# Optimization experiments

Hardware: AMD Instinct MI355X
Metric: run time of the kernel (lower is better)

## Reference

```python
import jax, jax.numpy as jnp
import numpy as np

DIM = 512
NUM_HEADS = 8
HEAD_DIM = DIM // NUM_HEADS
SOFT_CAP = 50.0
EPS = 1e-6
ROPE_BASE = 10000.0


def _rope_cos_sin(T):
    inv_freq = 1.0 / (ROPE_BASE ** (jnp.arange(0, HEAD_DIM, 2, dtype=jnp.float32) / HEAD_DIM))
    t = jnp.arange(T, dtype=jnp.float32)
    freqs = jnp.einsum('t,f->tf', t, inv_freq)            # (T, HEAD_DIM//2)
    emb = jnp.concatenate([freqs, freqs], axis=-1)         # (T, HEAD_DIM)
    return jnp.cos(emb), jnp.sin(emb)


def _rotate_half(x):
    x1, x2 = jnp.split(x, 2, axis=-1)
    return jnp.concatenate([-x2, x1], axis=-1)


def _apply_rope(x, cos, sin):
    # x: (B,H,T,hd); cos/sin: (T,hd) broadcast over B,H
    return x * cos + _rotate_half(x) * sin


def _rmsnorm(x, g):
    var = jnp.mean(jnp.square(x), axis=-1, keepdims=True)
    return x * jax.lax.rsqrt(var + EPS) * g


def setup_inputs() -> dict:
    key = jax.random.key(0)
    ks = jax.random.split(key, 7)
    B, T = 256, 256
    s = 1.0 / np.sqrt(DIM)
    return {
        'x': jax.random.normal(ks[0], (B, T, DIM), dtype=jnp.float32),
        'wq': jax.random.normal(ks[1], (DIM, DIM), dtype=jnp.float32) * s,
        'wk': jax.random.normal(ks[2], (DIM, DIM), dtype=jnp.float32) * s,
        'wv': jax.random.normal(ks[3], (DIM, DIM), dtype=jnp.float32) * s,
        'wo': jax.random.normal(ks[4], (DIM, DIM), dtype=jnp.float32) * s,
        'gq': jnp.ones((HEAD_DIM,), dtype=jnp.float32),
        'gk': jnp.ones((HEAD_DIM,), dtype=jnp.float32),
    }


def reference(x, wq, wk, wv, wo, gq, gk):
    B, T, D = x.shape
    H, hd = NUM_HEADS, HEAD_DIM
    scale = hd ** -0.5

    def proj(w):
        return jnp.einsum('btd,ed->bte', x, w).reshape(B, T, H, hd).transpose(0, 2, 1, 3)

    q = proj(wq)  # (B,H,T,hd)
    k = proj(wk)
    v = proj(wv)

    q = _rmsnorm(q, gq)
    k = _rmsnorm(k, gk)

    cos, sin = _rope_cos_sin(T)
    q = _apply_rope(q, cos, sin)
    k = _apply_rope(k, cos, sin)

    attn = jnp.einsum('bhqd,bhkd->bhqk', q, k) * scale
    attn = SOFT_CAP * jnp.tanh(attn / SOFT_CAP)
    causal = jnp.tril(jnp.ones((T, T), dtype=bool))
    attn = jnp.where(causal, attn, -jnp.inf)
    attn = jax.nn.softmax(attn.astype(jnp.float32), axis=-1).astype(v.dtype)

    out = jnp.einsum('bhqk,bhkd->bhqd', attn, v)
    out = out.transpose(0, 2, 1, 3).reshape(B, T, D)
    return jnp.einsum('btd,ed->bte', out, wo)
```

## Files before the change

kernel.cpp:

```cpp
#include <hip/hip_runtime.h>
#include <cstdint>
#include <cstddef>

#define B_   256
#define T_   256
#define D_   512
#define H_   8
#define HD_  64
#define BT_  65536
#define KDIM 512

typedef __bf16 bf16x8_t __attribute__((ext_vector_type(8)));
typedef __bf16 bf16x4_t __attribute__((ext_vector_type(4)));
typedef float  f32x4_t  __attribute__((ext_vector_type(4)));

__device__ __forceinline__ void gload16(const void* gp, void* lp) {
  __builtin_amdgcn_global_load_lds(
      (const __attribute__((address_space(1))) void*)gp,
      (__attribute__((address_space(3))) void*)lp, 16, 0, 0);
}

#define BAR()   __builtin_amdgcn_s_barrier()
#define SCB()   __builtin_amdgcn_sched_barrier(0)
#define LGKM0() asm volatile("s_waitcnt lgkmcnt(0)" ::: "memory")

__global__ __launch_bounds__(256) void prep(
    const float* __restrict__ x,
    const float* __restrict__ wq, const float* __restrict__ wk,
    const float* __restrict__ wv, const float* __restrict__ wo,
    __bf16* __restrict__ xb, __bf16* __restrict__ wb,
    float* __restrict__ rc, float* __restrict__ rs) {
  const int b = blockIdx.x;
  if (b < 2048) {
    for (size_t i = (size_t)b * 256 + threadIdx.x; i < 8388608UL; i += 524288UL) {
      f32x4_t v = *(const f32x4_t*)&x[i * 4];
      bf16x4_t o;
      o[0] = (__bf16)v[0]; o[1] = (__bf16)v[1]; o[2] = (__bf16)v[2]; o[3] = (__bf16)v[3];
      *(bf16x4_t*)&xb[i * 4] = o;
    }
  } else if (b < 2304) {
    for (int i = (b - 2048) * 256 + threadIdx.x; i < 262144; i += 65536) {
      int which = i >> 16;
      int off   = (i & 65535) * 4;
      const float* src = (which == 0) ? wq : (which == 1) ? wk : (which == 2) ? wv : wo;
      f32x4_t v = *(const f32x4_t*)&src[off];
      bf16x4_t o;
      o[0] = (__bf16)v[0]; o[1] = (__bf16)v[1]; o[2] = (__bf16)v[2]; o[3] = (__bf16)v[3];
      *(bf16x4_t*)&wb[(size_t)which * 262144 + off] = o;
    }
  } else {
    int idx = (b - 2304) * 256 + threadIdx.x;
    if (idx < T_ * 32) {
      int t = idx >> 5, j = idx & 31;
      float inv = powf(10000.f, -(float)j * (1.0f / 32.0f));
      float a = (float)t * inv;
      rc[idx] = cosf(a);
      rs[idx] = sinf(a);
    }
  }
}

template <int MODE>
__global__ __launch_bounds__(256, 2) void gemm256(
    const __bf16* __restrict__ A, const __bf16* __restrict__ W,
    void* __restrict__ outp) {
  __shared__ __bf16 lds[32768];
  const int tid = threadIdx.x;
  const int lane = tid & 63, w = tid >> 6;
  const int wm = w >> 1, wn = w & 1;
  const int l15 = lane & 15, lg = lane >> 4;
  const int swl = l15 & 7;

  const int cpx = gridDim.x >> 3;
  const int swz = (blockIdx.x & 7) * cpx + (blockIdx.x >> 3);
  int m_idx, bz, bx;
  if (MODE == 0) {
    m_idx = swz / 12;
    const int rem = swz - m_idx * 12;
    bz = rem >> 2;
    bx = rem & 3;
  } else {
    m_idx = swz >> 2;
    bz = 0;
    bx = swz & 3;
  }
  const int m0 = m_idx * 128, n0 = bx * 128;

  const __bf16* Ag = A + (size_t)m0 * KDIM;
  const __bf16* Bg = W + (size_t)bz * (KDIM * KDIM) + (size_t)n0 * KDIM;
  const int srow = tid >> 3;
  const int scol = (((tid & 7) ^ ((tid >> 3) & 7)) * 8);

#define STAGE(J) do {                                                        \
    const int T__ = (J) >> 2, r__ = (J) & 3;                                 \
    const int h__ = r__ >> 1;                                                \
    const int isB__ = (r__ == 1 || r__ == 2);                                \
    const size_t grow__ = (size_t)(h__ * 64 + srow) * KDIM + T__ * 64 + scol; \
    const __bf16* gp__ = isB__ ? (Bg + grow__) : (Ag + grow__);              \
    __bf16* lp__ = &lds[(T__ & 1) * 16384 + isB__ * 8192 + (h__ * 64 + w * 8) * 64]; \
    gload16(gp__, lp__);                                                     \
    gload16(gp__ + 32 * KDIM, lp__ + 32 * 64);                               \
  } while (0)

  f32x4_t acc[4][4];
#pragma unroll
  for (int i = 0; i < 4; i++)
#pragma unroll
    for (int j = 0; j < 4; j++) acc[i][j] = (f32x4_t){0.f, 0.f, 0.f, 0.f};

  bf16x8_t a0[2][2], a1[2][2], b0[2][2], b1[2][2];

#define PH_A(P, STJ) do {                                                    \
    const int ab__ = (P) * 16384;                                            \
    _Pragma("unroll") for (int i = 0; i < 2; i++)                            \
      _Pragma("unroll") for (int s = 0; s < 2; s++)                          \
        a0[i][s] = *(const bf16x8_t*)&lds[ab__ + (wm * 32 + i * 16 + l15) * 64 + (((s * 4 + lg) ^ swl) << 3)]; \
    _Pragma("unroll") for (int j = 0; j < 2; j++)                            \
      _Pragma("unroll") for (int s = 0; s < 2; s++)                          \
        b0[j][s] = *(const bf16x8_t*)&lds[ab__ + 8192 + (wn * 32 + j * 16 + l15) * 64 + (((s * 4 + lg) ^ swl) << 3)]; \
    if ((STJ) >= 0) STAGE(STJ);                                              \
    SCB(); BAR(); LGKM0(); SCB();                                            \
    __builtin_amdgcn_s_setprio(1);                                           \
    _Pragma("unroll") for (int i = 0; i < 2; i++)                            \
      _Pragma("unroll") for (int j = 0; j < 2; j++) {                        \
        acc[i][j] = __builtin_amdgcn_mfma_f32_16x16x32_bf16(a0[i][0], b0[j][0], acc[i][j], 0, 0, 0); \
        acc[i][j] = __builtin_amdgcn_mfma_f32_16x16x32_bf16(a0[i][1], b0[j][1], acc[i][j], 0, 0, 0); \
      }                                                                      \
    __builtin_amdgcn_s_setprio(0); SCB(); BAR();                             \
  } while (0)

#define PH_B(P, STJ) do {                                                    \
    const int ab__ = (P) * 16384;                                            \
    _Pragma("unroll") for (int j = 0; j < 2; j++)                            \
      _Pragma("unroll") for (int s = 0; s < 2; s++)                          \
        b1[j][s] = *(const bf16x8_t*)&lds[ab__ + 8192 + (64 + wn * 32 + j * 16 + l15) * 64 + (((s * 4 + lg) ^ swl) << 3)]; \
    if ((STJ) >= 0) STAGE(STJ);                                              \
    SCB(); BAR(); LGKM0(); SCB();                                            \
    __builtin_amdgcn_s_setprio(1);                                           \
    _Pragma("unroll") for (int i = 0; i < 2; i++)                            \
      _Pragma("unroll") for (int j = 0; j < 2; j++) {                        \
        acc[i][j + 2] = __builtin_amdgcn_mfma_f32_16x16x32_bf16(a0[i][0], b1[j][0], acc[i][j + 2], 0, 0, 0); \
        acc[i][j + 2] = __builtin_amdgcn_mfma_f32_16x16x32_bf16(a0[i][1], b1[j][1], acc[i][j + 2], 0, 0, 0); \
      }                                                                      \
    __builtin_amdgcn_s_setprio(0); SCB(); BAR();                             \
  } while (0)

#define PH_C(P, STJ) do {                                                    \
    const int ab__ = (P) * 16384;                                            \
    _Pragma("unroll") for (int i = 0; i < 2; i++)                            \
      _Pragma("unroll") for (int s = 0; s < 2; s++)                          \
        a1[i][s] = *(const bf16x8_t*)&lds[ab__ + (64 + wm * 32 + i * 16 + l15) * 64 + (((s * 4 + lg) ^ swl) << 3)]; \
    if ((STJ) >= 0) STAGE(STJ);                                              \
    SCB(); BAR(); LGKM0(); SCB();                                            \
    __builtin_amdgcn_s_setprio(1);                                           \
    _Pragma("unroll") for (int i = 0; i < 2; i++)                            \
      _Pragma("unroll") for (int j = 0; j < 2; j++) {                        \
        acc[i + 2][j + 2] = __builtin_amdgcn_mfma_f32_16x16x32_bf16(a1[i][0], b1[j][0], acc[i + 2][j + 2], 0, 0, 0); \
        acc[i + 2][j + 2] = __builtin_amdgcn_mfma_f32_16x16x32_bf16(a1[i][1], b1[j][1], acc[i + 2][j + 2], 0, 0, 0); \
      }                                                                      \
    __builtin_amdgcn_s_setprio(0); SCB(); BAR();                             \
  } while (0)

#define PH_D(P, STJ, VM) do {                                                \
    if ((STJ) >= 0) STAGE(STJ);                                              \
    SCB(); BAR();                                                            \
    __builtin_amdgcn_s_setprio(1);                                           \
    _Pragma("unroll") for (int i = 0; i < 2; i++)                            \
      _Pragma("unroll") for (int j = 0; j < 2; j++) {                        \
        acc[i + 2][j] = __builtin_amdgcn_mfma_f32_16x16x32_bf16(a1[i][0], b0[j][0], acc[i + 2][j], 0, 0, 0); \
        acc[i + 2][j] = __builtin_amdgcn_mfma_f32_16x16x32_bf16(a1[i][1], b0[j][1], acc[i + 2][j], 0, 0, 0); \
      }                                                                      \
    __builtin_amdgcn_s_setprio(0);                                           \
    if ((VM) == 6) asm volatile("s_waitcnt vmcnt(6)" ::: "memory");          \
    else if ((VM) == 0) asm volatile("s_waitcnt vmcnt(0)" ::: "memory");     \
    SCB(); BAR();                                                            \
  } while (0)

  STAGE(0); STAGE(1); STAGE(2); STAGE(3); STAGE(4); STAGE(5); STAGE(6);
  asm volatile("s_waitcnt vmcnt(6)" ::: "memory");
  SCB(); BAR();

#pragma unroll 1
  for (int tp = 0; tp < 3; ++tp) {
    const int g0 = tp * 8;
    PH_A(0, g0 + 7);  PH_B(0, g0 + 8);  PH_C(0, g0 + 9);  PH_D(0, g0 + 10, 6);
    PH_A(1, g0 + 11); PH_B(1, g0 + 12); PH_C(1, g0 + 13); PH_D(1, g0 + 14, 6);
  }
  PH_A(0, 31); PH_B(0, -1); PH_C(0, -1); PH_D(0, -1, 0);
  PH_A(1, -1); PH_B(1, -1); PH_C(1, -1); PH_D(1, -1, -1);

#undef PH_A
#undef PH_B
#undef PH_C
#undef PH_D
#undef STAGE

#pragma unroll
  for (int i = 0; i < 4; i++) {
#pragma unroll
    for (int rr = 0; rr < 4; rr++) {
      const int m = m0 + (i >> 1) * 64 + wm * 32 + (i & 1) * 16 + lg * 4 + rr;
      if (MODE == 0) {
        __bf16* outz = (__bf16*)outp + (size_t)bz * ((size_t)BT_ * D_);
        const int bb = m >> 8, tt = m & 255;
        const size_t rbase = ((size_t)bb * H_) * T_ * HD_ + (size_t)tt * HD_;
#pragma unroll
        for (int j = 0; j < 4; j++) {
          const int c = n0 + (j >> 1) * 64 + wn * 32 + (j & 1) * 16 + l15;
          const int hh = c >> 6, dd = c & 63;
          outz[rbase + (size_t)hh * (T_ * HD_) + dd] = (__bf16)acc[i][j][rr];
        }
      } else {
        float* outf = (float*)outp;
#pragma unroll
        for (int j = 0; j < 4; j++) {
          const int c = n0 + (j >> 1) * 64 + wn * 32 + (j & 1) * 16 + l15;
          outf[(size_t)m * D_ + c] = acc[i][j][rr];
        }
      }
    }
  }
}

__global__ __launch_bounds__(512, 2) void attn_kernel(
    const __bf16* __restrict__ qb, const __bf16* __restrict__ kb,
    const __bf16* __restrict__ vb, __bf16* __restrict__ ob,
    const float* __restrict__ gq, const float* __restrict__ gk,
    const float* __restrict__ rc, const float* __restrict__ rs) {
  __shared__ __bf16 Kl[256 * 64];
  __shared__ __bf16 VT[64 * 256];
  __shared__ __bf16 Pl[8 * 16 * 64];
  const int bh = blockIdx.x;
  const __bf16* Qg = qb + (size_t)bh * (T_ * HD_);
  const __bf16* Kg = kb + (size_t)bh * (T_ * HD_);
  const __bf16* Vg = vb + (size_t)bh * (T_ * HD_);
  const int tid = threadIdx.x, lane = tid & 63, w = tid >> 6;
  const int bI = bh >> 3, hI = bh & 7;

#pragma unroll
  for (int p = 0; p < 4; p++) {
    const int t = p * 64 + (tid >> 3);
    const int a = tid & 7;
    const int d0 = a * 8;
    bf16x8_t kv = *(const bf16x8_t*)&Kg[t * HD_ + d0];
    float kf[8], ss = 0.f;
#pragma unroll
    for (int j = 0; j < 8; j++) { kf[j] = (float)kv[j]; ss += kf[j] * kf[j]; }
    ss += __shfl_xor(ss, 1); ss += __shfl_xor(ss, 2); ss += __shfl_xor(ss, 4);
    const float rn = rsqrtf(ss * 0.015625f + 1e-6f);
    const f32x4_t gk0 = *(const f32x4_t*)&gk[d0];
    const f32x4_t gk1 = *(const f32x4_t*)&gk[d0 + 4];
    float vn[8];
#pragma unroll
    for (int j = 0; j < 8; j++) vn[j] = kf[j] * rn * ((j < 4) ? gk0[j] : gk1[j - 4]);
    float pn[8];
#pragma unroll
    for (int j = 0; j < 8; j++) pn[j] = __shfl_xor(vn[j], 4);
    const int f0 = (a & 3) * 8;
    const f32x4_t c0 = *(const f32x4_t*)&rc[t * 32 + f0];
    const f32x4_t c1 = *(const f32x4_t*)&rc[t * 32 + f0 + 4];
    const f32x4_t s0 = *(const f32x4_t*)&rs[t * 32 + f0];
    const f32x4_t s1 = *(const f32x4_t*)&rs[t * 32 + f0 + 4];
    const float sg = (a < 4) ? -1.f : 1.f;
    bf16x8_t ko;
#pragma unroll
    for (int j = 0; j < 8; j++) {
      const float cc = (j < 4) ? c0[j] : c1[j - 4];
      const float sS = (j < 4) ? s0[j] : s1[j - 4];
      ko[j] = (__bf16)(vn[j] * cc + sg * pn[j] * sS);
    }
    *(bf16x8_t*)&Kl[t * 64 + (((a ^ (t & 7)) << 3))] = ko;
    bf16x8_t vv = *(const bf16x8_t*)&Vg[t * HD_ + d0];
#pragma unroll
    for (int j = 0; j < 8; j++) {
      const int row = d0 + j;
      const int rk = (row & 7) ^ ((row >> 3) & 7);
      VT[row * 256 + (((t >> 3) ^ rk) << 3) + (t & 7)] = vv[j];
    }
  }
  __syncthreads();

  const int l15 = lane & 15;
  const int lg = lane >> 4;
  const int sw = l15 & 7;
  const f32x4_t zero = {0.f, 0.f, 0.f, 0.f};
  const float C1 = 0.0072134752f;
  const float LOG2E = 1.44269504f;

  for (int half = 0; half < 2; half++) {
    const int qt = half ? (15 - w) : w;
    const int q0 = qt * 16;
    const int tq = q0 + l15;
    bf16x8_t q0r = *(const bf16x8_t*)&Qg[tq * HD_ + lg * 8];
    bf16x8_t q1r = *(const bf16x8_t*)&Qg[tq * HD_ + 32 + lg * 8];
    float qf0[8], qf1[8], qss = 0.f;
#pragma unroll
    for (int j = 0; j < 8; j++) {
      qf0[j] = (float)q0r[j]; qf1[j] = (float)q1r[j];
      qss += qf0[j] * qf0[j] + qf1[j] * qf1[j];
    }
    qss += __shfl_xor(qss, 16); qss += __shfl_xor(qss, 32);
    const float qrn = rsqrtf(qss * 0.015625f + 1e-6f);
    const f32x4_t gqa = *(const f32x4_t*)&gq[lg * 8];
    const f32x4_t gqb2 = *(const f32x4_t*)&gq[lg * 8 + 4];
    const f32x4_t gqc = *(const f32x4_t*)&gq[32 + lg * 8];
    const f32x4_t gqd = *(const f32x4_t*)&gq[32 + lg * 8 + 4];
    const f32x4_t qc0 = *(const f32x4_t*)&rc[tq * 32 + lg * 8];
    const f32x4_t qc1 = *(const f32x4_t*)&rc[tq * 32 + lg * 8 + 4];
    const f32x4_t qs0 = *(const f32x4_t*)&rs[tq * 32 + lg * 8];
    const f32x4_t qs1 = *(const f32x4_t*)&rs[tq * 32 + lg * 8 + 4];
    bf16x8_t aq0, aq1;
#pragma unroll
    for (int j = 0; j < 8; j++) {
      const float glo = (j < 4) ? gqa[j] : gqb2[j - 4];
      const float ghi = (j < 4) ? gqc[j] : gqd[j - 4];
      const float cc  = (j < 4) ? qc0[j] : qc1[j - 4];
      const float sS  = (j < 4) ? qs0[j] : qs1[j - 4];
      const float vlo = qf0[j] * qrn * glo;
      const float vhi = qf1[j] * qrn * ghi;
      aq0[j] = (__bf16)(vlo * cc - vhi * sS);
      aq1[j] = (__bf16)(vhi * cc + vlo * sS);
    }

    const int ntiles_e = (qt + 2) & ~1;
    const int qr = q0 + (lg << 2);

    float ls = 0.f;
    f32x4_t o[4];
#pragma unroll
    for (int j = 0; j < 4; j++) o[j] = zero;

    for (int t0 = 0; t0 < ntiles_e; t0 += 4) {
      const int te = (t0 + 4 < ntiles_e) ? (t0 + 4) : ntiles_e;
      for (int n = t0; n < te; ++n) {
        bf16x8_t kb0 = *(const bf16x8_t*)&Kl[(n * 16 + l15) * 64 + ((lg ^ sw) << 3)];
        bf16x8_t kb1 = *(const bf16x8_t*)&Kl[(n * 16 + l15) * 64 + (((4 + lg) ^ sw) << 3)];
        __builtin_amdgcn_s_setprio(1);
        f32x4_t a = __builtin_amdgcn_mfma_f32_16x16x32_bf16(kb0, aq0, zero, 0, 0, 0);
        a = __builtin_amdgcn_mfma_f32_16x16x32_bf16(kb1, aq1, a, 0, 0, 0);
        __builtin_amdgcn_s_setprio(0);
        const int kbase = n * 16 + (lg << 2);
        bf16x4_t pk;
#pragma unroll
        for (int r = 0; r < 4; r++) {
          float e2 = __builtin_amdgcn_exp2f(a[r] * C1);
          float cm = -100.f * __builtin_amdgcn_rcpf(e2 + 1.f);
          float p = __builtin_amdgcn_exp2f(cm * LOG2E);
          p = (kbase + r <= tq) ? p : 0.f;
          ls += p;
          pk[r] = (__bf16)p;
        }
        const int nn = n - t0;
        const int ph = (2 * nn + (lg >> 1)) ^ sw;
        *(bf16x4_t*)&Pl[w * 1024 + l15 * 64 + ph * 8 + (lg & 1) * 4] = pk;
      }
      asm volatile("s_waitcnt lgkmcnt(0)" ::: "memory");
      __builtin_amdgcn_sched_barrier(0);
      const int nkc = (te - t0) >> 1;
      for (int kcc = 0; kcc < nkc; ++kcc) {
        const int phr = (kcc * 4 + lg) ^ sw;
        bf16x8_t pa = *(const bf16x8_t*)&Pl[w * 1024 + l15 * 64 + phr * 8];
        __builtin_amdgcn_s_setprio(1);
#pragma unroll
        for (int j = 0; j < 4; j++) {
          const int row = j * 16 + l15;
          const int rk = sw ^ ((2 * j + (l15 >> 3)) & 7);
          const int sl = (t0 << 1) + kcc * 4 + lg;
          bf16x8_t bv = *(const bf16x8_t*)&VT[row * 256 + ((sl ^ rk) << 3)];
          o[j] = __builtin_amdgcn_mfma_f32_16x16x32_bf16(pa, bv, o[j], 0, 0, 0);
        }
        __builtin_amdgcn_s_setprio(0);
      }
    }

    ls += __shfl_xor(ls, 16);
    ls += __shfl_xor(ls, 32);
    const float inv = 1.0f / ls;
    float rl[4];
#pragma unroll
    for (int r = 0; r < 4; r++) rl[r] = __shfl(inv, (lg << 2) + r);

#pragma unroll
    for (int j = 0; j < 4; j++) {
      int dd = j * 16 + l15;
#pragma unroll
      for (int r = 0; r < 4; r++) {
        int q = qr + r;
        ob[((size_t)(bI * T_ + q)) * D_ + hI * HD_ + dd] = (__bf16)(o[j][r] * rl[r]);
      }
    }
  }
}

extern "C" void kernel_launch(void* const* d_in, const int* in_sizes, int n_in,
                              void* d_out, int out_size, void* d_ws, size_t ws_size,
                              hipStream_t stream) {
  (void)in_sizes; (void)n_in; (void)out_size; (void)ws_size;
  const float* x  = (const float*)d_in[0];
  const float* wq = (const float*)d_in[1];
  const float* wk = (const float*)d_in[2];
  const float* wv = (const float*)d_in[3];
  const float* wo = (const float*)d_in[4];
  const float* gq = (const float*)d_in[5];
  const float* gk = (const float*)d_in[6];

  char* ws = (char*)d_ws;
  __bf16* xb   = (__bf16*)ws;
  __bf16* qkvb = (__bf16*)(ws + 67108864UL);
  __bf16* qb = qkvb;
  __bf16* kb = qkvb + 33554432UL;
  __bf16* vb = qkvb + 67108864UL;
  __bf16* wb = (__bf16*)(ws + 4UL * 67108864UL);
  float*  rc = (float*)(ws + 4UL * 67108864UL + 2097152UL);
  float*  rs = rc + 8192;
  __bf16* ob = xb;

  prep<<<dim3(2336), 256, 0, stream>>>(x, wq, wk, wv, wo, xb, wb, rc, rs);
  gemm256<0><<<dim3(6144), 256, 0, stream>>>(xb, wb, (void*)qkvb);
  attn_kernel<<<dim3(2048), 512, 0, stream>>>(qb, kb, vb, ob, gq, gk, rc, rs);
  gemm256<1><<<dim3(2048), 256, 0, stream>>>(ob, wb + 3UL * 262144UL, d_out);
}
```

Before: 290.1 us.

## Restructure GEMM mainloop to triple-buffered K=32 tiles with one barrier per step

Replaces the four-phase, double-buffered K=64 GEMM pipeline with a simpler triple-buffered K=32 pipeline. Each step issues one stage of global-to-LDS loads, reads full 4x4 fragments and runs 16 MFMAs, with a single barrier per iteration. LDS per block shrinks from 64KB to 48KB and launch bounds rise to 3 blocks per SM, aiming for more occupancy and fewer barriers. The trade-off is less load/compute interleaving inside a step, a different swizzle on 64-byte rows (possible bank conflicts) and more register pressure from the larger fragment set.

```diff
diff --git a/kernel.cpp b/kernel.cpp
--- a/kernel.cpp
+++ b/kernel.cpp
@@ -61,15 +61,14 @@
 }
 
 template <int MODE>
-__global__ __launch_bounds__(256, 2) void gemm256(
+__global__ __launch_bounds__(256, 3) void gemm256(
     const __bf16* __restrict__ A, const __bf16* __restrict__ W,
     void* __restrict__ outp) {
-  __shared__ __bf16 lds[32768];
+  __shared__ __bf16 lds[24576];
   const int tid = threadIdx.x;
   const int lane = tid & 63, w = tid >> 6;
   const int wm = w >> 1, wn = w & 1;
   const int l15 = lane & 15, lg = lane >> 4;
-  const int swl = l15 & 7;
 
   const int cpx = gridDim.x >> 3;
   const int swz = (blockIdx.x & 7) * cpx + (blockIdx.x >> 3);
@@ -88,18 +87,18 @@
 
   const __bf16* Ag = A + (size_t)m0 * KDIM;
   const __bf16* Bg = W + (size_t)bz * (KDIM * KDIM) + (size_t)n0 * KDIM;
-  const int srow = tid >> 3;
-  const int scol = (((tid & 7) ^ ((tid >> 3) & 7)) * 8);
-
-#define STAGE(J) do {                                                        \
-    const int T__ = (J) >> 2, r__ = (J) & 3;                                 \
-    const int h__ = r__ >> 1;                                                \
-    const int isB__ = (r__ == 1 || r__ == 2);                                \
-    const size_t grow__ = (size_t)(h__ * 64 + srow) * KDIM + T__ * 64 + scol; \
-    const __bf16* gp__ = isB__ ? (Bg + grow__) : (Ag + grow__);              \
-    __bf16* lp__ = &lds[(T__ & 1) * 16384 + isB__ * 8192 + (h__ * 64 + w * 8) * 64]; \
-    gload16(gp__, lp__);                                                     \
-    gload16(gp__ + 32 * KDIM, lp__ + 32 * 64);                               \
+  const int srow = tid >> 2;
+  const int scol = (((tid & 3) ^ ((tid >> 3) & 3)) * 8);
+
+#define STAGE(T) do {                                                        \
+    const int b3__ = (T) % 3;                                                \
+    __bf16* lb__ = &lds[b3__ * 8192];                                        \
+    const size_t g0__ = (size_t)srow * KDIM + (T) * 32 + scol;               \
+    const size_t g1__ = g0__ + (size_t)64 * KDIM;                            \
+    gload16(Ag + g0__, lb__ + tid * 8);                                      \
+    gload16(Ag + g1__, lb__ + 2048 + tid * 8);                               \
+    gload16(Bg + g0__, lb__ + 4096 + tid * 8);                               \
+    gload16(Bg + g1__, lb__ + 4096 + 2048 + tid * 8);                        \
   } while (0)
 
   f32x4_t acc[4][4];
@@ -108,105 +107,53 @@
 #pragma unroll
     for (int j = 0; j < 4; j++) acc[i][j] = (f32x4_t){0.f, 0.f, 0.f, 0.f};
 
-  bf16x8_t a0[2][2], a1[2][2], b0[2][2], b1[2][2];
-
-#define PH_A(P, STJ) do {                                                    \
-    const int ab__ = (P) * 16384;                                            \
-    _Pragma("unroll") for (int i = 0; i < 2; i++)                            \
-      _Pragma("unroll") for (int s = 0; s < 2; s++)                          \
-        a0[i][s] = *(const bf16x8_t*)&lds[ab__ + (wm * 32 + i * 16 + l15) * 64 + (((s * 4 + lg) ^ swl) << 3)]; \
-    _Pragma("unroll") for (int j = 0; j < 2; j++)                            \
-      _Pragma("unroll") for (int s = 0; s < 2; s++)                          \
-        b0[j][s] = *(const bf16x8_t*)&lds[ab__ + 8192 + (wn * 32 + j * 16 + l15) * 64 + (((s * 4 + lg) ^ swl) << 3)]; \
-    if ((STJ) >= 0) STAGE(STJ);                                              \
-    SCB(); BAR(); LGKM0(); SCB();                                            \
-    __builtin_amdgcn_s_setprio(1);                                           \
-    _Pragma("unroll") for (int i = 0; i < 2; i++)                            \
-      _Pragma("unroll") for (int j = 0; j < 2; j++) {                        \
-        acc[i][j] = __builtin_amdgcn_mfma_f32_16x16x32_bf16(a0[i][0], b0[j][0], acc[i][j], 0, 0, 0); \
-        acc[i][j] = __builtin_amdgcn_mfma_f32_16x16x32_bf16(a0[i][1], b0[j][1], acc[i][j], 0, 0, 0); \
-      }                                                                      \
-    __builtin_amdgcn_s_setprio(0); SCB(); BAR();                             \
-  } while (0)
-
-#define PH_B(P, STJ) do {                                                    \
-    const int ab__ = (P) * 16384;                                            \
-    _Pragma("unroll") for (int j = 0; j < 2; j++)                            \
-      _Pragma("unroll") for (int s = 0; s < 2; s++)                          \
-        b1[j][s] = *(const bf16x8_t*)&lds[ab__ + 8192 + (64 + wn * 32 + j * 16 + l15) * 64 + (((s * 4 + lg) ^ swl) << 3)]; \
-    if ((STJ) >= 0) STAGE(STJ);                                              \
-    SCB(); BAR(); LGKM0(); SCB();                                            \
-    __builtin_amdgcn_s_setprio(1);                                           \
-    _Pragma("unroll") for (int i = 0; i < 2; i++)                            \
-      _Pragma("unroll") for (int j = 0; j < 2; j++) {                        \
-        acc[i][j + 2] = __builtin_amdgcn_mfma_f32_16x16x32_bf16(a0[i][0], b1[j][0], acc[i][j + 2], 0, 0, 0); \
-        acc[i][j + 2] = __builtin_amdgcn_mfma_f32_16x16x32_bf16(a0[i][1], b1[j][1], acc[i][j + 2], 0, 0, 0); \
-      }                                                                      \
-    __builtin_amdgcn_s_setprio(0); SCB(); BAR();                             \
-  } while (0)
-
-#define PH_C(P, STJ) do {                                                    \
-    const int ab__ = (P) * 16384;                                            \
-    _Pragma("unroll") for (int i = 0; i < 2; i++)                            \
-      _Pragma("unroll") for (int s = 0; s < 2; s++)                          \
-        a1[i][s] = *(const bf16x8_t*)&lds[ab__ + (64 + wm * 32 + i * 16 + l15) * 64 + (((s * 4 + lg) ^ swl) << 3)]; \
-    if ((STJ) >= 0) STAGE(STJ);                                              \
-    SCB(); BAR(); LGKM0(); SCB();                                            \
-    __builtin_amdgcn_s_setprio(1);                                           \
-    _Pragma("unroll") for (int i = 0; i < 2; i++)                            \
-      _Pragma("unroll") for (int j = 0; j < 2; j++) {                        \
-        acc[i + 2][j + 2] = __builtin_amdgcn_mfma_f32_16x16x32_bf16(a1[i][0], b1[j][0], acc[i + 2][j + 2], 0, 0, 0); \
-        acc[i + 2][j + 2] = __builtin_amdgcn_mfma_f32_16x16x32_bf16(a1[i][1], b1[j][1], acc[i + 2][j + 2], 0, 0, 0); \
-      }                                                                      \
-    __builtin_amdgcn_s_setprio(0); SCB(); BAR();                             \
-  } while (0)
-
-#define PH_D(P, STJ, VM) do {                                                \
-    if ((STJ) >= 0) STAGE(STJ);                                              \
-    SCB(); BAR();                                                            \
-    __builtin_amdgcn_s_setprio(1);                                           \
-    _Pragma("unroll") for (int i = 0; i < 2; i++)                            \
-      _Pragma("unroll") for (int j = 0; j < 2; j++) {                        \
-        acc[i + 2][j] = __builtin_amdgcn_mfma_f32_16x16x32_bf16(a1[i][0], b0[j][0], acc[i + 2][j], 0, 0, 0); \
-        acc[i + 2][j] = __builtin_amdgcn_mfma_f32_16x16x32_bf16(a1[i][1], b0[j][1], acc[i + 2][j], 0, 0, 0); \
-      }                                                                      \
-    __builtin_amdgcn_s_setprio(0);                                           \
-    if ((VM) == 6) asm volatile("s_waitcnt vmcnt(6)" ::: "memory");          \
-    else if ((VM) == 0) asm volatile("s_waitcnt vmcnt(0)" ::: "memory");     \
-    SCB(); BAR();                                                            \
-  } while (0)
-
-  STAGE(0); STAGE(1); STAGE(2); STAGE(3); STAGE(4); STAGE(5); STAGE(6);
-  asm volatile("s_waitcnt vmcnt(6)" ::: "memory");
+  STAGE(0); STAGE(1);
+  asm volatile("s_waitcnt vmcnt(4)" ::: "memory");
   SCB(); BAR();
 
 #pragma unroll 1
-  for (int tp = 0; tp < 3; ++tp) {
-    const int g0 = tp * 8;
-    PH_A(0, g0 + 7);  PH_B(0, g0 + 8);  PH_C(0, g0 + 9);  PH_D(0, g0 + 10, 6);
-    PH_A(1, g0 + 11); PH_B(1, g0 + 12); PH_C(1, g0 + 13); PH_D(1, g0 + 14, 6);
-  }
-  PH_A(0, 31); PH_B(0, -1); PH_C(0, -1); PH_D(0, -1, 0);
-  PH_A(1, -1); PH_B(1, -1); PH_C(1, -1); PH_D(1, -1, -1);
-
-#undef PH_A
-#undef PH_B
-#undef PH_C
-#undef PH_D
+  for (int t = 0; t < 16; ++t) {
+    if (t < 14) STAGE(t + 2);
+    const int bb = (t % 3) * 8192;
+    bf16x8_t af[4], bf[4];
+#pragma unroll
+    for (int i = 0; i < 4; i++) {
+      const int R = wm * 64 + i * 16 + l15;
+      af[i] = *(const bf16x8_t*)&lds[bb + R * 32 + ((lg ^ ((R >> 1) & 3)) << 3)];
+    }
+#pragma unroll
+    for (int j = 0; j < 4; j++) {
+      const int R = wn * 64 + j * 16 + l15;
+      bf[j] = *(const bf16x8_t*)&lds[bb + 4096 + R * 32 + ((lg ^ ((R >> 1) & 3)) << 3)];
+    }
+    LGKM0(); SCB();
+    __builtin_amdgcn_s_setprio(1);
+#pragma unroll
+    for (int i = 0; i < 4; i++)
+#pragma unroll
+      for (int j = 0; j < 4; j++)
+        acc[i][j] = __builtin_amdgcn_mfma_f32_16x16x32_bf16(af[i], bf[j], acc[i][j], 0, 0, 0);
+    __builtin_amdgcn_s_setprio(0);
+    SCB();
+    if (t < 14) asm volatile("s_waitcnt vmcnt(4)" ::: "memory");
+    else if (t == 14) asm volatile("s_waitcnt vmcnt(0)" ::: "memory");
+    SCB(); BAR();
+  }
+
 #undef STAGE
 
 #pragma unroll
   for (int i = 0; i < 4; i++) {
 #pragma unroll
     for (int rr = 0; rr < 4; rr++) {
-      const int m = m0 + (i >> 1) * 64 + wm * 32 + (i & 1) * 16 + lg * 4 + rr;
+      const int m = m0 + wm * 64 + i * 16 + lg * 4 + rr;
       if (MODE == 0) {
         __bf16* outz = (__bf16*)outp + (size_t)bz * ((size_t)BT_ * D_);
-        const int bb = m >> 8, tt = m & 255;
-        const size_t rbase = ((size_t)bb * H_) * T_ * HD_ + (size_t)tt * HD_;
+        const int bb2 = m >> 8, tt = m & 255;
+        const size_t rbase = ((size_t)bb2 * H_) * T_ * HD_ + (size_t)tt * HD_;
 #pragma unroll
         for (int j = 0; j < 4; j++) {
-          const int c = n0 + (j >> 1) * 64 + wn * 32 + (j & 1) * 16 + l15;
+          const int c = n0 + wn * 64 + j * 16 + l15;
           const int hh = c >> 6, dd = c & 63;
           outz[rbase + (size_t)hh * (T_ * HD_) + dd] = (__bf16)acc[i][j][rr];
         }
@@ -214,7 +161,7 @@
         float* outf = (float*)outp;
 #pragma unroll
         for (int j = 0; j < 4; j++) {
-          const int c = n0 + (j >> 1) * 64 + wn * 32 + (j & 1) * 16 + l15;
+          const int c = n0 + wn * 64 + j * 16 + l15;
           outf[(size_t)m * D_ + c] = acc[i][j][rr];
         }
       }
```

Result: slower. 312.6 us (+7.7%).
